# Performance work log

Measured on AMD Instinct MI355X. Metric: run time of the kernel, lower is better.

## Reference

```python
import jax, jax.numpy as jnp
import numpy as np

B, N, L = 2, 2048, 2048
DQ, DKV, H, WF = 1024, 1024, 16, 4
HD = DQ // H
EPS = 1e-5


def _ln(x, g, b):
    m = jnp.mean(x, axis=-1, keepdims=True)
    v = jnp.mean(jnp.square(x - m), axis=-1, keepdims=True)
    return (x - m) * jax.lax.rsqrt(v + EPS) * g + b


def setup_inputs() -> dict:
    key = jax.random.key(0)
    ks = jax.random.split(key, 12)
    s = 0.02
    return {
        "x_q": jax.random.normal(ks[0], (B, N, DQ), jnp.float32),
        "x_kv": jax.random.normal(ks[1], (B, L, DKV), jnp.float32),
        "qn_g": jnp.ones((DQ,), jnp.float32),
        "qn_b": jnp.zeros((DQ,), jnp.float32),
        "kvn_g": jnp.ones((DKV,), jnp.float32),
        "kvn_b": jnp.zeros((DKV,), jnp.float32),
        "Wq": jax.random.normal(ks[2], (DQ, DQ), jnp.float32) * s,
        "bq": jnp.zeros((DQ,), jnp.float32),
        "Wk": jax.random.normal(ks[3], (DQ, DKV), jnp.float32) * s,
        "bk": jnp.zeros((DQ,), jnp.float32),
        "Wv": jax.random.normal(ks[4], (DQ, DKV), jnp.float32) * s,
        "bv": jnp.zeros((DQ,), jnp.float32),
        "Wo": jax.random.normal(ks[5], (DQ, DQ), jnp.float32) * s,
        "bo": jnp.zeros((DQ,), jnp.float32),
        "n2_g": jnp.ones((DQ,), jnp.float32),
        "n2_b": jnp.zeros((DQ,), jnp.float32),
        "W1": jax.random.normal(ks[6], (WF * DQ, DQ), jnp.float32) * s,
        "b1": jnp.zeros((WF * DQ,), jnp.float32),
        "W2": jax.random.normal(ks[7], (DQ, WF * DQ), jnp.float32) * s,
        "b2": jnp.zeros((DQ,), jnp.float32),
    }


def reference(x_q, x_kv, qn_g, qn_b, kvn_g, kvn_b, Wq, bq, Wk, bk, Wv, bv,
              Wo, bo, n2_g, n2_b, W1, b1, W2, b2):
    # projections (torch Linear: x @ W.T + b)
    q = (_ln(x_q, qn_g, qn_b) @ Wq.T + bq).reshape(B, N, H, HD)
    kvn = _ln(x_kv, kvn_g, kvn_b)
    k = (kvn @ Wk.T + bk).reshape(B, L, H, HD)
    v = (kvn @ Wv.T + bv).reshape(B, L, H, HD)

    # attention with softmax-1: exp(s)/(1 + sum exp(s)), numerically stable
    scale = 1.0 / jnp.sqrt(jnp.float32(HD))
    s = jnp.einsum("bnhd,blhd->bhnl", q, k) * scale  # [B,H,N,L]
    m = jnp.max(s, axis=-1, keepdims=True)
    m = jnp.maximum(m, 0.0)  # include the implicit zero logit of softmax-1
    p = jnp.exp(s - m)
    denom = jnp.sum(p, axis=-1, keepdims=True) + jnp.exp(-m)
    attn = p / denom
    attn_out = jnp.einsum("bhnl,blhd->bnhd", attn, v).reshape(B, N, DQ)

    # residual + out proj
    x = x_q + (attn_out @ Wo.T + bo)
    # residual MLP (GELU, exact/erf as torch nn.GELU default)
    h = jax.nn.gelu(_ln(x, n2_g, n2_b) @ W1.T + b1, approximate=False)
    x = x + (h @ W2.T + b2)
    return x
```

## Files before the change

kernel.cpp:

```cpp
#include <hip/hip_runtime.h>
#include <hip/hip_bf16.h>
#include <stdint.h>

#define DEV __device__ __forceinline__

typedef unsigned short ushort_t;
typedef __attribute__((ext_vector_type(8))) short bf16x8;
typedef __attribute__((ext_vector_type(4))) float f32x4;

DEV uint32_t f2bf2(float lo, float hi) {
  uint32_t d;
  asm("v_cvt_pk_bf16_f32 %0, %1, %2" : "=v"(d) : "v"(lo), "v"(hi));
  return d;
}
DEV ushort_t f2bf(float f) { return (ushort_t)f2bf2(f, f); }

DEV void gload_lds16(const void* gp, void* lp) {
  __builtin_amdgcn_global_load_lds(
      (__attribute__((address_space(1))) void*)(void*)(uintptr_t)gp,
      (__attribute__((address_space(3))) void*)lp, 16, 0, 0);
}

__global__ __launch_bounds__(256) void cvt_all(
    const float* __restrict__ Wq, const float* __restrict__ Wk,
    const float* __restrict__ Wv, const float* __restrict__ Wo,
    const float* __restrict__ W1, const float* __restrict__ W2,
    ushort_t* __restrict__ WQKVB, ushort_t* __restrict__ WoB,
    ushort_t* __restrict__ W1B, ushort_t* __restrict__ W2B) {
  int i = blockIdx.x * 256 + threadIdx.x;
  const float* src; ushort_t* dst; int j;
  if (i < 262144)            { src = Wq; dst = WQKVB;            j = i; }
  else if (i < 524288)       { src = Wk; dst = WQKVB + 1048576;  j = i - 262144; }
  else if (i < 786432)       { src = Wv; dst = WQKVB + 2097152;  j = i - 524288; }
  else if (i < 1048576)      { src = Wo; dst = WoB;              j = i - 786432; }
  else if (i < 2097152)      { src = W1; dst = W1B;              j = i - 1048576; }
  else                       { src = W2; dst = W2B;              j = i - 2097152; }
  float4 v = ((const float4*)src)[j];
  uint2 o; o.x = f2bf2(v.x, v.y); o.y = f2bf2(v.z, v.w);
  ((uint2*)dst)[j] = o;
}

DEV void ln_row(const float* __restrict__ x, const float* __restrict__ g,
                const float* __restrict__ be, ushort_t* __restrict__ out, int row) {
  const int t = threadIdx.x;
  const float4 v = ((const float4*)(x + (size_t)row * 1024))[t];
  float s = v.x + v.y + v.z + v.w;
  float sq = v.x * v.x + v.y * v.y + v.z * v.z + v.w * v.w;
#pragma unroll
  for (int d = 1; d < 64; d <<= 1) { s += __shfl_xor(s, d); sq += __shfl_xor(sq, d); }
  __shared__ float sm[8];
  const int w = t >> 6, lane = t & 63;
  if (lane == 0) { sm[w * 2] = s; sm[w * 2 + 1] = sq; }
  __syncthreads();
  s = sm[0] + sm[2] + sm[4] + sm[6];
  sq = sm[1] + sm[3] + sm[5] + sm[7];
  const float mean = s * (1.f / 1024.f);
  const float var = sq * (1.f / 1024.f) - mean * mean;
  const float rstd = rsqrtf(var + 1e-5f);
  const float4 gv = ((const float4*)g)[t];
  const float4 bv = ((const float4*)be)[t];
  uint2 o;
  o.x = f2bf2((v.x - mean) * rstd * gv.x + bv.x, (v.y - mean) * rstd * gv.y + bv.y);
  o.y = f2bf2((v.z - mean) * rstd * gv.z + bv.z, (v.w - mean) * rstd * gv.w + bv.w);
  ((uint2*)(out + (size_t)row * 1024))[t] = o;
}

__global__ __launch_bounds__(256) void ln_bf16(const float* __restrict__ x,
                                               const float* __restrict__ g,
                                               const float* __restrict__ be,
                                               ushort_t* __restrict__ out) {
  ln_row(x, g, be, out, blockIdx.x);
}

__global__ __launch_bounds__(256) void ln_fused(
    const float* __restrict__ x_q, const float* __restrict__ x_kv,
    const float* __restrict__ qg, const float* __restrict__ qb,
    const float* __restrict__ kg, const float* __restrict__ kb,
    ushort_t* __restrict__ oq, ushort_t* __restrict__ okv) {
  const int r = blockIdx.x;
  if (r < 4096) ln_row(x_q, qg, qb, oq, r);
  else ln_row(x_kv, kg, kb, okv, r - 4096);
}

DEV void xcd_remap(int gx, int gy, int& bx, int& by) {
  const int lin = by * gx + bx;
  const int xcd = lin & 7, s = lin >> 3;
  by = xcd * (gy >> 3) + s / gx;
  bx = s % gx;
}

enum { EPI_BF16 = 0, EPI_KV = 1, EPI_RESID = 2, EPI_GELU = 3, EPI_QKV = 4 };

template <int BM, int TN, int BK, int EPI>
__global__ __launch_bounds__(256, (BM == 64) ? 4 : 3) void gemm_bt(
    const ushort_t* __restrict__ A,
    const ushort_t* __restrict__ A2,
    const ushort_t* __restrict__ Wb,
    const float* __restrict__ bias, const float* __restrict__ bias2,
    const float* __restrict__ bias3,
    const float* __restrict__ resid,
    void* __restrict__ outp, void* __restrict__ outp2, void* __restrict__ outp3,
    int M, int N, int K, float oscale) {
  constexpr int WAVES_N = (TN == 128 || BM == 64) ? 2 : 1;
  constexpr int WAVES_M = 4 / WAVES_N;
  constexpr int NI = BM / WAVES_M / 16;
  constexpr int NJ = TN / WAVES_N / 16;
  constexpr int CH = BK / 8;
  constexpr int NA = (BM * CH) / 256;
  constexpr int NBL = (TN * CH) / 256;
  constexpr int KS = BK / 32;
  __shared__ ushort_t As[2][BM * BK];
  __shared__ ushort_t Bs[2][TN * BK];
  const int t = threadIdx.x;
  const int w = t >> 6, lane = t & 63;
  const int qd = lane >> 4, ql = lane & 15;
  int bx = blockIdx.x, by = blockIdx.y;
  xcd_remap(gridDim.x, gridDim.y, bx, by);
  const int m0 = by * BM, n0 = bx * TN;
  const int wm = (w / WAVES_N) * (BM / WAVES_M);
  const int wn = (w % WAVES_N) * (TN / WAVES_N);
  const int sw = (BK == 64) ? (ql & 7) : ((ql >> 1) & 3);

  const ushort_t* Ause = (EPI == EPI_QKV && n0 >= 1024) ? A2 : A;

  const ushort_t* pa[NA];
#pragma unroll
  for (int p = 0; p < NA; p++) {
    int n = p * 256 + t, row = n / CH, c = n % CH;
    int g = (BK == 64) ? (c ^ (row & 7)) : (c ^ ((row >> 1) & 3));
    pa[p] = Ause + (size_t)(m0 + row) * K + g * 8;
  }
  const ushort_t* pb[NBL];
#pragma unroll
  for (int p = 0; p < NBL; p++) {
    int n = p * 256 + t, row = n / CH, c = n % CH;
    int g = (BK == 64) ? (c ^ (row & 7)) : (c ^ ((row >> 1) & 3));
    pb[p] = Wb + (size_t)(n0 + row) * K + g * 8;
  }

#pragma unroll
  for (int p = 0; p < NA; p++) { gload_lds16(pa[p], &As[0][(p * 256 + t) * 8]); pa[p] += BK; }
#pragma unroll
  for (int p = 0; p < NBL; p++) { gload_lds16(pb[p], &Bs[0][(p * 256 + t) * 8]); pb[p] += BK; }
  __syncthreads();

  f32x4 acc[NI][NJ] = {};
  const int NIT = K / BK;
  int cur = 0;

  for (int it = 0; it < NIT; ++it) {
    if (it + 1 < NIT) {
#pragma unroll
      for (int p = 0; p < NA; p++) { gload_lds16(pa[p], &As[1 ^ cur][(p * 256 + t) * 8]); pa[p] += BK; }
#pragma unroll
      for (int p = 0; p < NBL; p++) { gload_lds16(pb[p], &Bs[1 ^ cur][(p * 256 + t) * 8]); pb[p] += BK; }
    }
    const ushort_t* Ac = As[cur];
    const ushort_t* Bc = Bs[cur];
#pragma unroll
    for (int ks = 0; ks < KS; ks++) {
      bf16x8 af[NI], bf[NJ];
#pragma unroll
      for (int i = 0; i < NI; i++)
        af[i] = *(const bf16x8*)&Ac[(wm + i * 16 + ql) * BK + ((ks * 4 + qd) ^ sw) * 8];
#pragma unroll
      for (int j = 0; j < NJ; j++)
        bf[j] = *(const bf16x8*)&Bc[(wn + j * 16 + ql) * BK + ((ks * 4 + qd) ^ sw) * 8];
#pragma unroll
      for (int i = 0; i < NI; i++)
#pragma unroll
        for (int j = 0; j < NJ; j++)
          acc[i][j] = __builtin_amdgcn_mfma_f32_16x16x32_bf16(af[i], bf[j], acc[i][j], 0, 0, 0);
    }
    __syncthreads();
    cur ^= 1;
  }

#pragma unroll
  for (int i = 0; i < NI; i++) {
    const int mr = m0 + wm + i * 16 + qd * 4;
#pragma unroll
    for (int j = 0; j < NJ; j++) {
      const int col = n0 + wn + j * 16 + ql;
      f32x4 v = acc[i][j];
      if constexpr (EPI == EPI_BF16) {
        const float bb = bias[col];
        ushort_t* o = (ushort_t*)outp;
#pragma unroll
        for (int r = 0; r < 4; r++) o[(size_t)(mr + r) * N + col] = f2bf((v[r] + bb) * oscale);
      } else if constexpr (EPI == EPI_QKV) {
        if (col < 1024) {
          const float bb = bias[col];
          ushort_t* o = (ushort_t*)outp;
#pragma unroll
          for (int r = 0; r < 4; r++) o[(size_t)(mr + r) * 1024 + col] = f2bf((v[r] + bb) * oscale);
        } else if (col < 2048) {
          const int c2 = col - 1024;
          const float bb = bias2[c2];
          ushort_t* o = (ushort_t*)outp2;
#pragma unroll
          for (int r = 0; r < 4; r++) o[(size_t)(mr + r) * 1024 + c2] = f2bf(v[r] + bb);
        } else {
          const int vc = col - 2048;
          const float bb = bias3[vc];
          const int h = vc >> 6, d = vc & 63;
          const int b = mr >> 11, l0 = mr & 2047;
          uint2 pk;
          pk.x = f2bf2(v[0] + bb, v[1] + bb);
          pk.y = f2bf2(v[2] + bb, v[3] + bb);
          *(uint2*)((ushort_t*)outp3 + ((((size_t)b * 16 + h) * 64 + d) * 2048 + l0)) = pk;
        }
      } else if constexpr (EPI == EPI_RESID) {
        const float bb = bias[col];
        float* o = (float*)outp;
#pragma unroll
        for (int r = 0; r < 4; r++) {
          size_t idx = (size_t)(mr + r) * N + col;
          o[idx] = resid[idx] + v[r] + bb;
        }
      } else if constexpr (EPI == EPI_GELU) {
        const float bb = bias[col];
        ushort_t* o = (ushort_t*)outp;
#pragma unroll
        for (int r = 0; r < 4; r++) {
          float x = v[r] + bb;
          float gx = 0.5f * x * (1.0f + erff(x * 0.70710678118654752f));
          o[(size_t)(mr + r) * N + col] = f2bf(gx);
        }
      }
    }
  }
}

__global__ __launch_bounds__(256, 2) void flash_attn(const ushort_t* __restrict__ Qg,
                                                     const ushort_t* __restrict__ Kg,
                                                     const ushort_t* __restrict__ VTg,
                                                     ushort_t* __restrict__ Og) {
  __shared__ ushort_t QPs[128 * 64];
  __shared__ ushort_t Ks[2][64 * 64];
  __shared__ ushort_t Vs[2][64 * 64];
  const int t = threadIdx.x, w = t >> 6, lane = t & 63;
  const int qd = lane >> 4, ql = lane & 15;
  int bx = blockIdx.x, bh = blockIdx.y;
  xcd_remap(gridDim.x, gridDim.y, bx, bh);
  const int b = bh >> 4, h = bh & 15;
  const int n0 = bx * 128;
  const ushort_t* Qp = Qg + ((size_t)b * 2048 + n0) * 1024 + h * 64;
  const ushort_t* Kp = Kg + (size_t)b * 2048 * 1024 + h * 64;
  const ushort_t* Vp = VTg + (size_t)bh * 64 * 2048;
  const int sw = ql & 7;

  const ushort_t* kp2[2];
  const ushort_t* vp2[2];
#pragma unroll
  for (int p = 0; p < 2; p++) {
    int n = p * 256 + t, row = n >> 3, c = (n & 7) ^ (row & 7);
    kp2[p] = Kp + (size_t)row * 1024 + c * 8;
    vp2[p] = Vp + (size_t)row * 2048 + c * 8;
  }

#pragma unroll
  for (int p = 0; p < 4; p++) {
    int n = p * 256 + t, row = n >> 3, c = (n & 7) ^ (row & 7);
    gload_lds16(Qp + (size_t)row * 1024 + c * 8, &QPs[n * 8]);
  }
#pragma unroll
  for (int p = 0; p < 2; p++) {
    int n = p * 256 + t;
    gload_lds16(kp2[p], &Ks[0][n * 8]);
    gload_lds16(vp2[p], &Vs[0][n * 8]);
    kp2[p] += 64 * 1024;
    vp2[p] += 64;
  }
  __syncthreads();

  bf16x8 aq[2][2];
#pragma unroll
  for (int i = 0; i < 2; i++)
#pragma unroll
    for (int ks = 0; ks < 2; ks++)
      aq[i][ks] = *(const bf16x8*)&QPs[(w * 32 + i * 16 + ql) * 64 + ((ks * 4 + qd) ^ sw) * 8];
  __syncthreads();

  f32x4 accO[2][4] = {};
  float lro2[2] = {0.f, 0.f};

  int cur = 0;
  for (int lt = 0; lt < 32; ++lt) {
    if (lt + 1 < 32) {
#pragma unroll
      for (int p = 0; p < 2; p++) {
        int n = p * 256 + t;
        gload_lds16(kp2[p], &Ks[1 ^ cur][n * 8]);
        gload_lds16(vp2[p], &Vs[1 ^ cur][n * 8]);
        kp2[p] += 64 * 1024;
        vp2[p] += 64;
      }
    }
    const ushort_t* Kc = Ks[cur];
    const ushort_t* Vc = Vs[cur];

    f32x4 accS[4][2] = {};
#pragma unroll
    for (int ks = 0; ks < 2; ks++) {
      bf16x8 bk[4];
#pragma unroll
      for (int j = 0; j < 4; j++)
        bk[j] = *(const bf16x8*)&Kc[(j * 16 + ql) * 64 + ((ks * 4 + qd) ^ sw) * 8];
#pragma unroll
      for (int j = 0; j < 4; j++)
#pragma unroll
        for (int i = 0; i < 2; i++)
          accS[j][i] = __builtin_amdgcn_mfma_f32_16x16x32_bf16(bk[j], aq[i][ks], accS[j][i], 0, 0, 0);
    }

#pragma unroll
    for (int j = 0; j < 4; j++)
#pragma unroll
      for (int i = 0; i < 2; i++) {
        f32x4 p;
#pragma unroll
        for (int r = 0; r < 4; r++) {
          p[r] = __builtin_amdgcn_exp2f(accS[j][i][r]);
          lro2[i] += p[r];
        }
        const int n = w * 32 + i * 16 + ql;
        const int coff = (((j * 2 + (qd >> 1)) ^ sw) << 3) + ((qd & 1) << 2);
        uint2 pk; pk.x = f2bf2(p[0], p[1]); pk.y = f2bf2(p[2], p[3]);
        *(uint2*)&QPs[n * 64 + coff] = pk;
      }

#pragma unroll
    for (int ks = 0; ks < 2; ks++) {
      bf16x8 ap[2], bv[4];
#pragma unroll
      for (int i = 0; i < 2; i++)
        ap[i] = *(const bf16x8*)&QPs[(w * 32 + i * 16 + ql) * 64 + ((ks * 4 + qd) ^ sw) * 8];
#pragma unroll
      for (int jo = 0; jo < 4; jo++)
        bv[jo] = *(const bf16x8*)&Vc[(jo * 16 + ql) * 64 + ((ks * 4 + qd) ^ sw) * 8];
#pragma unroll
      for (int i = 0; i < 2; i++)
#pragma unroll
        for (int jo = 0; jo < 4; jo++)
          accO[i][jo] = __builtin_amdgcn_mfma_f32_16x16x32_bf16(ap[i], bv[jo], accO[i][jo], 0, 0, 0);
    }

    __syncthreads();
    cur ^= 1;
  }

  float dn[2];
#pragma unroll
  for (int i = 0; i < 2; i++) {
    float l = lro2[i];
    l += __shfl_xor(l, 16);
    l += __shfl_xor(l, 32);
    dn[i] = l + 1.0f;
  }

#pragma unroll
  for (int i = 0; i < 2; i++)
#pragma unroll
    for (int r = 0; r < 4; r++) {
      const float inv = 1.0f / __shfl(dn[i], qd * 4 + r);
      const int row = n0 + w * 32 + i * 16 + qd * 4 + r;
#pragma unroll
      for (int jo = 0; jo < 4; jo++)
        Og[((size_t)b * 2048 + row) * 1024 + h * 64 + jo * 16 + ql] =
            f2bf(accO[i][jo][r] * inv);
    }
}

extern "C" void kernel_launch(void* const* d_in, const int* in_sizes, int n_in,
                              void* d_out, int out_size, void* d_ws, size_t ws_size,
                              hipStream_t stream) {
  const float* x_q = (const float*)d_in[0];
  const float* x_kv = (const float*)d_in[1];
  const float* qn_g = (const float*)d_in[2];
  const float* qn_b = (const float*)d_in[3];
  const float* kvn_g = (const float*)d_in[4];
  const float* kvn_b = (const float*)d_in[5];
  const float* Wq = (const float*)d_in[6];
  const float* bq = (const float*)d_in[7];
  const float* Wk = (const float*)d_in[8];
  const float* bk = (const float*)d_in[9];
  const float* Wv = (const float*)d_in[10];
  const float* bv = (const float*)d_in[11];
  const float* Wo = (const float*)d_in[12];
  const float* bo = (const float*)d_in[13];
  const float* n2_g = (const float*)d_in[14];
  const float* n2_b = (const float*)d_in[15];
  const float* W1 = (const float*)d_in[16];
  const float* b1 = (const float*)d_in[17];
  const float* W2 = (const float*)d_in[18];
  const float* b2 = (const float*)d_in[19];

  char* ws = (char*)d_ws;
  const size_t MB = 1ull << 20;
  ushort_t* WQKVB = (ushort_t*)(ws + 0 * MB);
  ushort_t* WoB = (ushort_t*)(ws + 6 * MB);
  ushort_t* W1B = (ushort_t*)(ws + 8 * MB);
  ushort_t* W2B = (ushort_t*)(ws + 16 * MB);
  ushort_t* LNQ = (ushort_t*)(ws + 24 * MB);
  ushort_t* LNKV = (ushort_t*)(ws + 32 * MB);
  ushort_t* Qb = (ushort_t*)(ws + 40 * MB);
  ushort_t* Kb = (ushort_t*)(ws + 48 * MB);
  ushort_t* VTb = (ushort_t*)(ws + 56 * MB);
  ushort_t* AOb = (ushort_t*)(ws + 64 * MB);
  float* Xf = (float*)(ws + 72 * MB);
  ushort_t* LN2 = (ushort_t*)(ws + 88 * MB);
  ushort_t* Hb = (ushort_t*)(ws + 24 * MB);

  const float QSCALE = 0.18033688011112042f;

  cvt_all<<<12288, 256, 0, stream>>>(Wq, Wk, Wv, Wo, W1, W2, WQKVB, WoB, W1B, W2B);
  ln_fused<<<8192, 256, 0, stream>>>(x_q, x_kv, qn_g, qn_b, kvn_g, kvn_b, LNQ, LNKV);

  gemm_bt<128, 128, 32, EPI_QKV><<<dim3(24, 32), 256, 0, stream>>>(
      LNQ, LNKV, WQKVB, bq, bk, bv, nullptr, Qb, Kb, VTb, 4096, 3072, 1024, QSCALE);

  flash_attn<<<dim3(16, 32), 256, 0, stream>>>(Qb, Kb, VTb, AOb);

  gemm_bt<64, 64, 64, EPI_RESID><<<dim3(16, 64), 256, 0, stream>>>(
      AOb, nullptr, WoB, bo, nullptr, nullptr, x_q, Xf, nullptr, nullptr,
      4096, 1024, 1024, 1.0f);
  ln_bf16<<<4096, 256, 0, stream>>>(Xf, n2_g, n2_b, LN2);
  gemm_bt<128, 128, 32, EPI_GELU><<<dim3(32, 32), 256, 0, stream>>>(
      LN2, nullptr, W1B, b1, nullptr, nullptr, nullptr, Hb, nullptr, nullptr,
      4096, 4096, 1024, 1.0f);
  gemm_bt<64, 64, 64, EPI_RESID><<<dim3(16, 64), 256, 0, stream>>>(
      Hb, nullptr, W2B, b2, nullptr, nullptr, Xf, (float*)d_out, nullptr, nullptr,
      4096, 1024, 4096, 1.0f);
}
```

Before: 361.1 us.

## Add triple-buffered LDS pipeline with explicit vmcnt waits to 128x128 GEMMs

Adds a TRI template option to the bf16 GEMM. It uses three LDS buffers, prefetches two K-tiles ahead, and uses manual s_waitcnt vmcnt counts with raw s_barrier in place of __syncthreads. This lets the 128x128 QKV and W1 GEMMs keep more global loads in flight, hiding memory latency. The cost is 50% more LDS per block, which may lower occupancy below the launch-bounds target of 3 blocks, and the hand-written vmcnt immediates are tied to exactly 4 loads per tile.

After: 373.7 us. 1.03x slower.

```diff
diff --git a/kernel.cpp b/kernel.cpp
--- a/kernel.cpp
+++ b/kernel.cpp
@@ -91,7 +91,7 @@
 
 enum { EPI_BF16 = 0, EPI_KV = 1, EPI_RESID = 2, EPI_GELU = 3, EPI_QKV = 4 };
 
-template <int BM, int TN, int BK, int EPI>
+template <int BM, int TN, int BK, int EPI, int TRI>
 __global__ __launch_bounds__(256, (BM == 64) ? 4 : 3) void gemm_bt(
     const ushort_t* __restrict__ A,
     const ushort_t* __restrict__ A2,
@@ -109,8 +109,10 @@
   constexpr int NA = (BM * CH) / 256;
   constexpr int NBL = (TN * CH) / 256;
   constexpr int KS = BK / 32;
-  __shared__ ushort_t As[2][BM * BK];
-  __shared__ ushort_t Bs[2][TN * BK];
+  constexpr int NBUF = TRI ? 3 : 2;
+  static_assert(!TRI || (NA + NBL == 4), "vmcnt immediates assume 4 loads/tile");
+  __shared__ ushort_t As[NBUF][BM * BK];
+  __shared__ ushort_t Bs[NBUF][TN * BK];
   const int t = threadIdx.x;
   const int w = t >> 6, lane = t & 63;
   const int qd = lane >> 4, ql = lane & 15;
@@ -138,42 +140,90 @@
     pb[p] = Wb + (size_t)(n0 + row) * K + g * 8;
   }
 
-#pragma unroll
-  for (int p = 0; p < NA; p++) { gload_lds16(pa[p], &As[0][(p * 256 + t) * 8]); pa[p] += BK; }
-#pragma unroll
-  for (int p = 0; p < NBL; p++) { gload_lds16(pb[p], &Bs[0][(p * 256 + t) * 8]); pb[p] += BK; }
-  __syncthreads();
-
   f32x4 acc[NI][NJ] = {};
   const int NIT = K / BK;
-  int cur = 0;
-
-  for (int it = 0; it < NIT; ++it) {
-    if (it + 1 < NIT) {
-#pragma unroll
-      for (int p = 0; p < NA; p++) { gload_lds16(pa[p], &As[1 ^ cur][(p * 256 + t) * 8]); pa[p] += BK; }
-#pragma unroll
-      for (int p = 0; p < NBL; p++) { gload_lds16(pb[p], &Bs[1 ^ cur][(p * 256 + t) * 8]); pb[p] += BK; }
-    }
-    const ushort_t* Ac = As[cur];
-    const ushort_t* Bc = Bs[cur];
-#pragma unroll
-    for (int ks = 0; ks < KS; ks++) {
-      bf16x8 af[NI], bf[NJ];
-#pragma unroll
-      for (int i = 0; i < NI; i++)
-        af[i] = *(const bf16x8*)&Ac[(wm + i * 16 + ql) * BK + ((ks * 4 + qd) ^ sw) * 8];
-#pragma unroll
-      for (int j = 0; j < NJ; j++)
-        bf[j] = *(const bf16x8*)&Bc[(wn + j * 16 + ql) * BK + ((ks * 4 + qd) ^ sw) * 8];
-#pragma unroll
-      for (int i = 0; i < NI; i++)
+
+#pragma unroll
+  for (int p = 0; p < NA; p++) { gload_lds16(pa[p], &As[0][(p * 256 + t) * 8]); pa[p] += BK; }
+#pragma unroll
+  for (int p = 0; p < NBL; p++) { gload_lds16(pb[p], &Bs[0][(p * 256 + t) * 8]); pb[p] += BK; }
+  if constexpr (TRI) {
+#pragma unroll
+    for (int p = 0; p < NA; p++) { gload_lds16(pa[p], &As[1][(p * 256 + t) * 8]); pa[p] += BK; }
+#pragma unroll
+    for (int p = 0; p < NBL; p++) { gload_lds16(pb[p], &Bs[1][(p * 256 + t) * 8]); pb[p] += BK; }
+  }
+  __syncthreads();
+
+  if constexpr (TRI) {
+    int rb = 0, sb = 2;
+    for (int it = 0; it < NIT; ++it) {
+      if (it + 2 < NIT) {
+#pragma unroll
+        for (int p = 0; p < NA; p++) { gload_lds16(pa[p], &As[sb][(p * 256 + t) * 8]); pa[p] += BK; }
+#pragma unroll
+        for (int p = 0; p < NBL; p++) { gload_lds16(pb[p], &Bs[sb][(p * 256 + t) * 8]); pb[p] += BK; }
+        asm volatile("s_waitcnt vmcnt(8)" ::: "memory");
+      } else if (it + 1 < NIT) {
+        asm volatile("s_waitcnt vmcnt(4)" ::: "memory");
+      } else {
+        asm volatile("s_waitcnt vmcnt(0)" ::: "memory");
+      }
+      __builtin_amdgcn_sched_barrier(0);
+      __builtin_amdgcn_s_barrier();
+      __builtin_amdgcn_sched_barrier(0);
+      const ushort_t* Ac = As[rb];
+      const ushort_t* Bc = Bs[rb];
+#pragma unroll
+      for (int ks = 0; ks < KS; ks++) {
+        bf16x8 af[NI], bf[NJ];
+#pragma unroll
+        for (int i = 0; i < NI; i++)
+          af[i] = *(const bf16x8*)&Ac[(wm + i * 16 + ql) * BK + ((ks * 4 + qd) ^ sw) * 8];
 #pragma unroll
         for (int j = 0; j < NJ; j++)
-          acc[i][j] = __builtin_amdgcn_mfma_f32_16x16x32_bf16(af[i], bf[j], acc[i][j], 0, 0, 0);
-    }
-    __syncthreads();
-    cur ^= 1;
+          bf[j] = *(const bf16x8*)&Bc[(wn + j * 16 + ql) * BK + ((ks * 4 + qd) ^ sw) * 8];
+#pragma unroll
+        for (int i = 0; i < NI; i++)
+#pragma unroll
+          for (int j = 0; j < NJ; j++)
+            acc[i][j] = __builtin_amdgcn_mfma_f32_16x16x32_bf16(af[i], bf[j], acc[i][j], 0, 0, 0);
+      }
+      __builtin_amdgcn_sched_barrier(0);
+      __builtin_amdgcn_s_barrier();
+      __builtin_amdgcn_sched_barrier(0);
+      rb = (rb == 2) ? 0 : rb + 1;
+      sb = (sb == 2) ? 0 : sb + 1;
+    }
+  } else {
+    int cur = 0;
+    for (int it = 0; it < NIT; ++it) {
+      if (it + 1 < NIT) {
+#pragma unroll
+        for (int p = 0; p < NA; p++) { gload_lds16(pa[p], &As[1 ^ cur][(p * 256 + t) * 8]); pa[p] += BK; }
+#pragma unroll
+        for (int p = 0; p < NBL; p++) { gload_lds16(pb[p], &Bs[1 ^ cur][(p * 256 + t) * 8]); pb[p] += BK; }
+      }
+      const ushort_t* Ac = As[cur];
+      const ushort_t* Bc = Bs[cur];
+#pragma unroll
+      for (int ks = 0; ks < KS; ks++) {
+        bf16x8 af[NI], bf[NJ];
+#pragma unroll
+        for (int i = 0; i < NI; i++)
+          af[i] = *(const bf16x8*)&Ac[(wm + i * 16 + ql) * BK + ((ks * 4 + qd) ^ sw) * 8];
+#pragma unroll
+        for (int j = 0; j < NJ; j++)
+          bf[j] = *(const bf16x8*)&Bc[(wn + j * 16 + ql) * BK + ((ks * 4 + qd) ^ sw) * 8];
+#pragma unroll
+        for (int i = 0; i < NI; i++)
+#pragma unroll
+          for (int j = 0; j < NJ; j++)
+            acc[i][j] = __builtin_amdgcn_mfma_f32_16x16x32_bf16(af[i], bf[j], acc[i][j], 0, 0, 0);
+      }
+      __syncthreads();
+      cur ^= 1;
+    }
   }
 
 #pragma unroll
@@ -417,19 +467,19 @@
   cvt_all<<<12288, 256, 0, stream>>>(Wq, Wk, Wv, Wo, W1, W2, WQKVB, WoB, W1B, W2B);
   ln_fused<<<8192, 256, 0, stream>>>(x_q, x_kv, qn_g, qn_b, kvn_g, kvn_b, LNQ, LNKV);
 
-  gemm_bt<128, 128, 32, EPI_QKV><<<dim3(24, 32), 256, 0, stream>>>(
+  gemm_bt<128, 128, 32, EPI_QKV, 1><<<dim3(24, 32), 256, 0, stream>>>(
       LNQ, LNKV, WQKVB, bq, bk, bv, nullptr, Qb, Kb, VTb, 4096, 3072, 1024, QSCALE);
 
   flash_attn<<<dim3(16, 32), 256, 0, stream>>>(Qb, Kb, VTb, AOb);
 
-  gemm_bt<64, 64, 64, EPI_RESID><<<dim3(16, 64), 256, 0, stream>>>(
+  gemm_bt<64, 64, 64, EPI_RESID, 0><<<dim3(16, 64), 256, 0, stream>>>(
       AOb, nullptr, WoB, bo, nullptr, nullptr, x_q, Xf, nullptr, nullptr,
       4096, 1024, 1024, 1.0f);
   ln_bf16<<<4096, 256, 0, stream>>>(Xf, n2_g, n2_b, LN2);
-  gemm_bt<128, 128, 32, EPI_GELU><<<dim3(32, 32), 256, 0, stream>>>(
+  gemm_bt<128, 128, 32, EPI_GELU, 1><<<dim3(32, 32), 256, 0, stream>>>(
       LN2, nullptr, W1B, b1, nullptr, nullptr, nullptr, Hb, nullptr, nullptr,
       4096, 4096, 1024, 1.0f);
-  gemm_bt<64, 64, 64, EPI_RESID><<<dim3(16, 64), 256, 0, stream>>>(
+  gemm_bt<64, 64, 64, EPI_RESID, 0><<<dim3(16, 64), 256, 0, stream>>>(
       Hb, nullptr, W2B, b2, nullptr, nullptr, Xf, (float*)d_out, nullptr, nullptr,
       4096, 1024, 4096, 1.0f);
 }
```

## Add 256x256 pipelined GEMM kernel for W1 GELU projection and raise MFMA priority

Applied to the files above, without the earlier changes.

Adds a new 512-thread GEMM kernel with 256x256 output tiles, K=64 double-buffered LDS tiles, and quarter-stepped global-to-LDS loads interleaved with MFMA quadrants using explicit waitcnt and barriers. It replaces the 128x128 gemm_bt for the W1+GELU projection to raise data reuse per tile and overlap loads with compute. It also wraps MFMA blocks in flash attention and the new kernel with s_setprio to favour matrix issue. The large LDS footprint (128KB) and the 256-block grid reduce occupancy and wave-level parallelism on the device.

Result: slower. 368.5 us (+2.0%).

```diff
diff --git a/kernel.cpp b/kernel.cpp
--- a/kernel.cpp
+++ b/kernel.cpp
@@ -232,6 +232,174 @@
   }
 }
 
+template <int EPI>
+__global__ __launch_bounds__(512, 2) void gemm256(
+    const ushort_t* __restrict__ A, const ushort_t* __restrict__ A2,
+    const ushort_t* __restrict__ Wb,
+    const float* __restrict__ bias, const float* __restrict__ bias2,
+    const float* __restrict__ bias3,
+    void* __restrict__ outp, void* __restrict__ outp2, void* __restrict__ outp3,
+    int M, int N, int K, float oscale) {
+  __shared__ ushort_t As[2][256 * 64];
+  __shared__ ushort_t Bs[2][256 * 64];
+  const int t = threadIdx.x;
+  const int w = t >> 6, lane = t & 63;
+  const int qd = lane >> 4, ql = lane & 15;
+  const int wr = w >> 2, wc = w & 3;
+  int bx = blockIdx.x, by = blockIdx.y;
+  xcd_remap(gridDim.x, gridDim.y, bx, by);
+  const int m0 = by * 256, n0 = bx * 256;
+  const int sw = ql & 7;
+  const ushort_t* Ause = (EPI == EPI_QKV && n0 >= 1024) ? A2 : A;
+
+  const ushort_t* pa[4];
+  const ushort_t* pb[4];
+#pragma unroll
+  for (int p = 0; p < 4; p++) {
+    const int rl = p * 64 + (t >> 3);
+    const int cc = (t & 7) ^ (rl & 7);
+    const int la = ((rl & 64) << 1) | ((rl & 128) >> 1) | (rl & 63);
+    const int lb = ((rl & 128) >> 2) | ((rl & 96) << 1) | (rl & 31);
+    pa[p] = Ause + (size_t)(m0 + la) * K + cc * 8;
+    pb[p] = Wb + (size_t)(n0 + lb) * K + cc * 8;
+  }
+
+  gload_lds16(pa[0], &As[0][(0 * 512 + t) * 8]); pa[0] += 64;
+  gload_lds16(pa[1], &As[0][(1 * 512 + t) * 8]); pa[1] += 64;
+  gload_lds16(pb[0], &Bs[0][(0 * 512 + t) * 8]); pb[0] += 64;
+  gload_lds16(pb[1], &Bs[0][(1 * 512 + t) * 8]); pb[1] += 64;
+  gload_lds16(pb[2], &Bs[0][(2 * 512 + t) * 8]); pb[2] += 64;
+  gload_lds16(pb[3], &Bs[0][(3 * 512 + t) * 8]); pb[3] += 64;
+  gload_lds16(pa[2], &As[0][(2 * 512 + t) * 8]); pa[2] += 64;
+  gload_lds16(pa[3], &As[0][(3 * 512 + t) * 8]); pa[3] += 64;
+
+  f32x4 acc[8][4] = {};
+  const int NT = K / 64;
+  int cur = 0;
+
+  for (int T = 0; T < NT; ++T) {
+    const ushort_t* Ac = As[cur];
+    const ushort_t* Bc = Bs[cur];
+    ushort_t* An = As[cur ^ 1];
+    ushort_t* Bn = Bs[cur ^ 1];
+    const bool st = (T + 1 < NT);
+
+#define QUAD(MH, NH)                                                                     \
+    {                                                                                    \
+      bf16x8 af[4][2], bfr[2][2];                                                        \
+      _Pragma("unroll") for (int ii = 0; ii < 4; ii++)                                   \
+        _Pragma("unroll") for (int ks = 0; ks < 2; ks++)                                 \
+          af[ii][ks] = *(const bf16x8*)&Ac[((MH) * 128 + wr * 64 + ii * 16 + ql) * 64 +  \
+                                           ((ks * 4 + qd) ^ sw) * 8];                    \
+      _Pragma("unroll") for (int jj = 0; jj < 2; jj++)                                   \
+        _Pragma("unroll") for (int ks = 0; ks < 2; ks++)                                 \
+          bfr[jj][ks] = *(const bf16x8*)&Bc[((NH) * 128 + wc * 32 + jj * 16 + ql) * 64 + \
+                                            ((ks * 4 + qd) ^ sw) * 8];                   \
+      __builtin_amdgcn_s_setprio(1);                                                     \
+      _Pragma("unroll") for (int ii = 0; ii < 4; ii++)                                   \
+        _Pragma("unroll") for (int jj = 0; jj < 2; jj++)                                 \
+          _Pragma("unroll") for (int ks = 0; ks < 2; ks++)                               \
+            acc[(MH) * 4 + ii][(NH) * 2 + jj] = __builtin_amdgcn_mfma_f32_16x16x32_bf16( \
+                af[ii][ks], bfr[jj][ks], acc[(MH) * 4 + ii][(NH) * 2 + jj], 0, 0, 0);    \
+      __builtin_amdgcn_s_setprio(0);                                                     \
+    }
+
+    if (st) {
+      gload_lds16(pa[0], &An[(0 * 512 + t) * 8]); pa[0] += 64;
+      gload_lds16(pa[1], &An[(1 * 512 + t) * 8]); pa[1] += 64;
+      asm volatile("s_waitcnt vmcnt(6)" ::: "memory");
+    } else {
+      asm volatile("s_waitcnt vmcnt(4)" ::: "memory");
+    }
+    __builtin_amdgcn_sched_barrier(0);
+    __builtin_amdgcn_s_barrier();
+    __builtin_amdgcn_sched_barrier(0);
+    QUAD(0, 0)
+
+    if (st) {
+      gload_lds16(pb[0], &Bn[(0 * 512 + t) * 8]); pb[0] += 64;
+      gload_lds16(pb[1], &Bn[(1 * 512 + t) * 8]); pb[1] += 64;
+      asm volatile("s_waitcnt vmcnt(6)" ::: "memory");
+    } else {
+      asm volatile("s_waitcnt vmcnt(2)" ::: "memory");
+    }
+    __builtin_amdgcn_sched_barrier(0);
+    __builtin_amdgcn_s_barrier();
+    __builtin_amdgcn_sched_barrier(0);
+    QUAD(0, 1)
+
+    if (st) {
+      gload_lds16(pb[2], &Bn[(2 * 512 + t) * 8]); pb[2] += 64;
+      gload_lds16(pb[3], &Bn[(3 * 512 + t) * 8]); pb[3] += 64;
+      asm volatile("s_waitcnt vmcnt(6)" ::: "memory");
+    } else {
+      asm volatile("s_waitcnt vmcnt(0)" ::: "memory");
+    }
+    __builtin_amdgcn_sched_barrier(0);
+    __builtin_amdgcn_s_barrier();
+    __builtin_amdgcn_sched_barrier(0);
+    QUAD(1, 0)
+
+    if (st) {
+      gload_lds16(pa[2], &An[(2 * 512 + t) * 8]); pa[2] += 64;
+      gload_lds16(pa[3], &An[(3 * 512 + t) * 8]); pa[3] += 64;
+    }
+    __builtin_amdgcn_sched_barrier(0);
+    __builtin_amdgcn_s_barrier();
+    __builtin_amdgcn_sched_barrier(0);
+    QUAD(1, 1)
+#undef QUAD
+    cur ^= 1;
+  }
+
+#pragma unroll
+  for (int i = 0; i < 8; i++) {
+    const int mr = m0 + wr * 128 + i * 16 + qd * 4;
+#pragma unroll
+    for (int j = 0; j < 4; j++) {
+      const int col = n0 + wc * 64 + j * 16 + ql;
+      f32x4 v = acc[i][j];
+      if constexpr (EPI == EPI_GELU) {
+        const float bb = bias[col];
+        ushort_t* o = (ushort_t*)outp;
+#pragma unroll
+        for (int r = 0; r < 4; r++) {
+          float x = v[r] + bb;
+          float gx = 0.5f * x * (1.0f + erff(x * 0.70710678118654752f));
+          o[(size_t)(mr + r) * N + col] = f2bf(gx);
+        }
+      } else if constexpr (EPI == EPI_QKV) {
+        if (col < 1024) {
+          const float bb = bias[col];
+          ushort_t* o = (ushort_t*)outp;
+#pragma unroll
+          for (int r = 0; r < 4; r++) o[(size_t)(mr + r) * 1024 + col] = f2bf((v[r] + bb) * oscale);
+        } else if (col < 2048) {
+          const int c2 = col - 1024;
+          const float bb = bias2[c2];
+          ushort_t* o = (ushort_t*)outp2;
+#pragma unroll
+          for (int r = 0; r < 4; r++) o[(size_t)(mr + r) * 1024 + c2] = f2bf(v[r] + bb);
+        } else {
+          const int vc = col - 2048;
+          const float bb = bias3[vc];
+          const int h = vc >> 6, d = vc & 63;
+          const int b = mr >> 11, l0 = mr & 2047;
+          uint2 pk;
+          pk.x = f2bf2(v[0] + bb, v[1] + bb);
+          pk.y = f2bf2(v[2] + bb, v[3] + bb);
+          *(uint2*)((ushort_t*)outp3 + ((((size_t)b * 16 + h) * 64 + d) * 2048 + l0)) = pk;
+        }
+      } else if constexpr (EPI == EPI_BF16) {
+        const float bb = bias[col];
+        ushort_t* o = (ushort_t*)outp;
+#pragma unroll
+        for (int r = 0; r < 4; r++) o[(size_t)(mr + r) * N + col] = f2bf((v[r] + bb) * oscale);
+      }
+    }
+  }
+}
+
 __global__ __launch_bounds__(256, 2) void flash_attn(const ushort_t* __restrict__ Qg,
                                                      const ushort_t* __restrict__ Kg,
                                                      const ushort_t* __restrict__ VTg,
@@ -307,11 +475,13 @@
 #pragma unroll
       for (int j = 0; j < 4; j++)
         bk[j] = *(const bf16x8*)&Kc[(j * 16 + ql) * 64 + ((ks * 4 + qd) ^ sw) * 8];
+      __builtin_amdgcn_s_setprio(1);
 #pragma unroll
       for (int j = 0; j < 4; j++)
 #pragma unroll
         for (int i = 0; i < 2; i++)
           accS[j][i] = __builtin_amdgcn_mfma_f32_16x16x32_bf16(bk[j], aq[i][ks], accS[j][i], 0, 0, 0);
+      __builtin_amdgcn_s_setprio(0);
     }
 
 #pragma unroll
@@ -339,11 +509,13 @@
 #pragma unroll
       for (int jo = 0; jo < 4; jo++)
         bv[jo] = *(const bf16x8*)&Vc[(jo * 16 + ql) * 64 + ((ks * 4 + qd) ^ sw) * 8];
+      __builtin_amdgcn_s_setprio(1);
 #pragma unroll
       for (int i = 0; i < 2; i++)
 #pragma unroll
         for (int jo = 0; jo < 4; jo++)
           accO[i][jo] = __builtin_amdgcn_mfma_f32_16x16x32_bf16(ap[i], bv[jo], accO[i][jo], 0, 0, 0);
+      __builtin_amdgcn_s_setprio(0);
     }
 
     __syncthreads();
@@ -426,8 +598,8 @@
       AOb, nullptr, WoB, bo, nullptr, nullptr, x_q, Xf, nullptr, nullptr,
       4096, 1024, 1024, 1.0f);
   ln_bf16<<<4096, 256, 0, stream>>>(Xf, n2_g, n2_b, LN2);
-  gemm_bt<128, 128, 32, EPI_GELU><<<dim3(32, 32), 256, 0, stream>>>(
-      LN2, nullptr, W1B, b1, nullptr, nullptr, nullptr, Hb, nullptr, nullptr,
+  gemm256<EPI_GELU><<<dim3(16, 16), 512, 0, stream>>>(
+      LN2, nullptr, W1B, b1, nullptr, nullptr, Hb, nullptr, nullptr,
       4096, 4096, 1024, 1.0f);
   gemm_bt<64, 64, 64, EPI_RESID><<<dim3(16, 64), 256, 0, stream>>>(
       Hb, nullptr, W2B, b2, nullptr, nullptr, Xf, (float*)d_out, nullptr, nullptr,
```
